# Kernel tuning notes

Measured on AMD Instinct MI355X. Metric: run time of the kernel, lower is better.

Reference implementation:

```python
import jax, jax.numpy as jnp
import numpy as np

N_NODES = 100000
N_EDGES = 1600000
IN_DIM = 512
OUT_DIM = 64


def setup_inputs() -> dict:
    key = jax.random.key(0)
    k1, k2, k3 = jax.random.split(key, 3)
    x = jax.random.normal(k1, (N_NODES, IN_DIM), dtype=jnp.float32)
    edge_index = jax.random.randint(k2, (2, N_EDGES), 0, N_NODES, dtype=jnp.int64)
    # Glorot-ish init for the GCNConv linear weight, stored as [in, out]
    W = jax.random.normal(k3, (IN_DIM, OUT_DIM), dtype=jnp.float32) * (1.0 / np.sqrt(IN_DIM))
    b = jnp.zeros((OUT_DIM,), dtype=jnp.float32)
    return {"x": x, "edge_index": edge_index, "W": W, "b": b}


def reference(x, edge_index, W, b):
    N = x.shape[0]
    # --- gcn_norm: add self-loops, symmetric degree normalization ---
    loop = jnp.arange(N, dtype=edge_index.dtype)
    src = jnp.concatenate([edge_index[0], loop])  # message sources
    dst = jnp.concatenate([edge_index[1], loop])  # aggregation targets
    deg = jax.ops.segment_sum(jnp.ones_like(dst, dtype=x.dtype), dst, num_segments=N)
    deg_inv_sqrt = jnp.where(deg > 0, jax.lax.rsqrt(jnp.maximum(deg, 1.0)), 0.0)
    norm = deg_inv_sqrt[src] * deg_inv_sqrt[dst]  # [E+N]
    # --- linear transform then gather-scale-scatter aggregation ---
    h = x @ W                                   # [N, out]
    msg = h[src] * norm[:, None]                # [E+N, out]
    out = jax.ops.segment_sum(msg, dst, num_segments=N) + b
    return jax.nn.log_softmax(out, axis=1)
```

## Files before the change

### kernel.cpp

```cpp
#include <hip/hip_runtime.h>
#include <math.h>

#define N_NODES 100000
#define N_EDGES 1600000
#define IN_DIM 512
#define OUT_DIM 64
#define NB 1024
#define NPB 128
#define CHUNK (N_EDGES / NPB)
#define N_BUCKETS_USED 782
#define N_TILES (N_NODES / 16)
#define GEMM_WAVES 4096

typedef __attribute__((ext_vector_type(8))) short short8;
typedef __attribute__((ext_vector_type(4))) float float4v;

__device__ __forceinline__ unsigned short f2bf(float f) {
    unsigned int u = __float_as_uint(f);
    u += 0x7fffu + ((u >> 16) & 1u);
    return (unsigned short)(u >> 16);
}
__device__ __forceinline__ float bf2f(unsigned short s) {
    return __uint_as_float(((unsigned int)s) << 16);
}
__device__ __forceinline__ short8 cvt8(float4v lo, float4v hi) {
    union { short8 s8; unsigned short us[8]; } af;
    af.us[0] = f2bf(lo.x); af.us[1] = f2bf(lo.y);
    af.us[2] = f2bf(lo.z); af.us[3] = f2bf(lo.w);
    af.us[4] = f2bf(hi.x); af.us[5] = f2bf(hi.y);
    af.us[6] = f2bf(hi.z); af.us[7] = f2bf(hi.w);
    return af.s8;
}

__global__ __launch_bounds__(256) void k_hist1(const int* __restrict__ dst,
                                               int* __restrict__ blockHist) {
    __shared__ int hist[NB];
    const int t = threadIdx.x, b = blockIdx.x;
    for (int k = t; k < NB; k += 256) hist[k] = 0;
    __syncthreads();
    const int e0 = b * CHUNK;
    for (int i = t; i < CHUNK; i += 256)
        atomicAdd(&hist[dst[e0 + i] >> 7], 1);
    __syncthreads();
    for (int k = t; k < NB; k += 256) blockHist[b * NB + k] = hist[k];
}

__global__ __launch_bounds__(256) void k_offsets(const int* __restrict__ blockHist,
                                                 int* __restrict__ blockStart,
                                                 int* __restrict__ bucketBase) {
    __shared__ int colsum[NB];
    __shared__ int bbase[NB + 1];
    __shared__ int wtot[4];
    const int t = threadIdx.x, lane = t & 63, w = t >> 6;
    for (int k = t; k < NB; k += 256) {
        int s = 0;
        for (int b = 0; b < NPB; ++b) s += blockHist[b * NB + k];
        colsum[k] = s;
    }
    __syncthreads();
    int c0 = colsum[t * 4 + 0], c1 = colsum[t * 4 + 1];
    int c2 = colsum[t * 4 + 2], c3 = colsum[t * 4 + 3];
    int tsum = c0 + c1 + c2 + c3;
    int incl = tsum;
#pragma unroll
    for (int off = 1; off < 64; off <<= 1) {
        int u = __shfl_up(incl, off, 64);
        if (lane >= off) incl += u;
    }
    if (lane == 63) wtot[w] = incl;
    __syncthreads();
    int woff = 0;
#pragma unroll
    for (int k2 = 0; k2 < 4; ++k2) if (k2 < w) woff += wtot[k2];
    int excl = woff + incl - tsum;
    bbase[t * 4 + 0] = excl;
    bbase[t * 4 + 1] = excl + c0;
    bbase[t * 4 + 2] = excl + c0 + c1;
    bbase[t * 4 + 3] = excl + c0 + c1 + c2;
    if (t == 255) bbase[NB] = excl + tsum;
    __syncthreads();
    for (int k = t; k < NB + 1; k += 256) bucketBase[k] = bbase[k];
    for (int k = t; k < NB; k += 256) {
        int run = bbase[k];
        for (int b = 0; b < NPB; ++b) {
            blockStart[b * NB + k] = run;
            run += blockHist[b * NB + k];
        }
    }
}

__global__ __launch_bounds__(256) void k_partition(const int* __restrict__ dst,
                                                   const int* __restrict__ src,
                                                   const int* __restrict__ blockStart,
                                                   int* __restrict__ parts) {
    __shared__ int cursor[NB];
    const int t = threadIdx.x, b = blockIdx.x;
    for (int k = t; k < NB; k += 256) cursor[k] = blockStart[b * NB + k];
    __syncthreads();
    const int e0 = b * CHUNK;
    for (int i = t; i < CHUNK; i += 256) {
        int d = dst[e0 + i];
        int s = src[e0 + i];
        int k = d >> 7;
        int pos = atomicAdd(&cursor[k], 1);
        parts[pos] = ((d & 127) << 17) | s;
    }
}

__global__ __launch_bounds__(256) void k_bucket(const int* __restrict__ parts,
                                                const int* __restrict__ bucketBase,
                                                int* __restrict__ degi,
                                                int* __restrict__ row_ptr,
                                                int* __restrict__ csr) {
    __shared__ int cnt[128];
    __shared__ int cur[128];
    __shared__ int wtot[2];
    const int t = threadIdx.x, k = blockIdx.x;
    const int base = bucketBase[k];
    const int n    = bucketBase[k + 1] - base;
    if (t < 128) cnt[t] = 0;
    __syncthreads();
    for (int i = t; i < n; i += 256)
        atomicAdd(&cnt[parts[base + i] >> 17], 1);
    __syncthreads();
    int incl = 0, v = 0;
    if (t < 128) {
        int lane = t & 63;
        v = cnt[t];
        incl = v;
#pragma unroll
        for (int off = 1; off < 64; off <<= 1) {
            int u = __shfl_up(incl, off, 64);
            if (lane >= off) incl += u;
        }
        if (lane == 63) wtot[t >> 6] = incl;
    }
    __syncthreads();
    if (t < 128) {
        int excl = incl - v + ((t >> 6) ? wtot[0] : 0);
        cur[t] = excl;
        int node = k * 128 + t;
        if (node < N_NODES) {
            degi[node]    = v;
            row_ptr[node] = base + excl;
        }
    }
    __syncthreads();
    for (int i = t; i < n; i += 256) {
        int code = parts[base + i];
        int nl = code >> 17, s = code & 0x1FFFF;
        int pos = atomicAdd(&cur[nl], 1);
        csr[base + pos] = s;
    }
}

__global__ __launch_bounds__(256) void k_wswz(const float* __restrict__ W,
                                              unsigned short* __restrict__ Wswz) {
    int t = blockIdx.x * 256 + threadIdx.x;
    if (t < IN_DIM * OUT_DIM) {
        int k = t >> 6, n = t & 63;
        int kt = k >> 5, kin = k & 31;
        int quad = kin >> 3, j = kin & 7;
        int ct = n >> 4, l16 = n & 15;
        int lane = quad * 16 + l16;
        Wswz[(((kt * 4 + ct) * 64 + lane) * 8) + j] = f2bf(W[t]);
    }
}

__global__ __launch_bounds__(512, 2) void k_gemm(const float* __restrict__ x,
                                              const unsigned short* __restrict__ Wswz,
                                              const int* __restrict__ degi,
                                              unsigned short* __restrict__ h) {
    __shared__ short8 Wlds[64][64];
    const int t = threadIdx.x;
    {
        const float4v* s = (const float4v*)Wswz;
        float4v* d = (float4v*)Wlds;
        for (int i = t; i < 4096; i += 512) d[i] = s[i];
    }
    __syncthreads();

    const int lane = t & 63;
    const int quad = lane >> 4, l16 = lane & 15;
    const int wid = blockIdx.x * 8 + (t >> 6);

    const int t0 = (int)(((long)wid * N_TILES) / GEMM_WAVES);
    const int t1 = (int)(((long)(wid + 1) * N_TILES) / GEMM_WAVES);

    for (int tile = t0; tile < t1; ++tile) {
        const int r0 = tile * 16;
        const float* xrow = x + (size_t)(r0 + l16) * IN_DIM + quad * 8;

        float4v plo[4], phi[4];
#pragma unroll
        for (int kt = 0; kt < 4; ++kt) {
            plo[kt] = *(const float4v*)(xrow + kt * 32);
            phi[kt] = *(const float4v*)(xrow + kt * 32 + 4);
        }
        float4v acc[4] = {{0.f,0.f,0.f,0.f},{0.f,0.f,0.f,0.f},
                          {0.f,0.f,0.f,0.f},{0.f,0.f,0.f,0.f}};

#pragma unroll 1
        for (int kq = 0; kq < 4; ++kq) {
            short8 A[4];
#pragma unroll
            for (int kt = 0; kt < 4; ++kt) A[kt] = cvt8(plo[kt], phi[kt]);
            if (kq < 3) {
#pragma unroll
                for (int kt = 0; kt < 4; ++kt) {
                    plo[kt] = *(const float4v*)(xrow + (kq + 1) * 128 + kt * 32);
                    phi[kt] = *(const float4v*)(xrow + (kq + 1) * 128 + kt * 32 + 4);
                }
            }
#pragma unroll
            for (int kt = 0; kt < 4; ++kt) {
#pragma unroll
                for (int ct = 0; ct < 4; ++ct) {
                    short8 bf = Wlds[(kq * 4 + kt) * 4 + ct][lane];
                    acc[ct] = __builtin_amdgcn_mfma_f32_16x16x32_bf16(A[kt], bf, acc[ct], 0, 0, 0);
                }
            }
        }

#pragma unroll
        for (int reg = 0; reg < 4; ++reg) {
            int orow = r0 + quad * 4 + reg;
            float dinv = rsqrtf((float)(degi[orow] + 1));
#pragma unroll
            for (int ct = 0; ct < 4; ++ct)
                h[(size_t)orow * OUT_DIM + ct * 16 + l16] = f2bf(acc[ct][reg] * dinv);
        }
    }
}

__global__ __launch_bounds__(256) void k_gather(const int* __restrict__ degi,
                                                const int* __restrict__ row_ptr,
                                                const int* __restrict__ csr,
                                                const unsigned short* __restrict__ h,
                                                const float* __restrict__ b,
                                                float* __restrict__ out) {
    int node = blockIdx.x * 4 + (threadIdx.x >> 6);
    int lane = threadIdx.x & 63;
    if (node >= N_NODES) return;
    int cnt  = __builtin_amdgcn_readfirstlane(degi[node]);
    int base = __builtin_amdgcn_readfirstlane(row_ptr[node]);

    float acc = bf2f(h[(size_t)node * OUT_DIM + lane]);
    int e = 0;
    for (; e + 8 <= cnt; e += 8) {
        int s0 = csr[base + e + 0], s1 = csr[base + e + 1];
        int s2 = csr[base + e + 2], s3 = csr[base + e + 3];
        int s4 = csr[base + e + 4], s5 = csr[base + e + 5];
        int s6 = csr[base + e + 6], s7 = csr[base + e + 7];
        float v0 = bf2f(h[(size_t)s0 * OUT_DIM + lane]);
        float v1 = bf2f(h[(size_t)s1 * OUT_DIM + lane]);
        float v2 = bf2f(h[(size_t)s2 * OUT_DIM + lane]);
        float v3 = bf2f(h[(size_t)s3 * OUT_DIM + lane]);
        float v4 = bf2f(h[(size_t)s4 * OUT_DIM + lane]);
        float v5 = bf2f(h[(size_t)s5 * OUT_DIM + lane]);
        float v6 = bf2f(h[(size_t)s6 * OUT_DIM + lane]);
        float v7 = bf2f(h[(size_t)s7 * OUT_DIM + lane]);
        acc += ((v0 + v1) + (v2 + v3)) + ((v4 + v5) + (v6 + v7));
    }
    for (; e < cnt; ++e)
        acc += bf2f(h[(size_t)csr[base + e] * OUT_DIM + lane]);

    float v = acc * rsqrtf((float)(cnt + 1)) + b[lane];
    float m = v;
#pragma unroll
    for (int off = 32; off > 0; off >>= 1) m = fmaxf(m, __shfl_xor(m, off, 64));
    float ex = expf(v - m);
    float s = ex;
#pragma unroll
    for (int off = 32; off > 0; off >>= 1) s += __shfl_xor(s, off, 64);
    out[(size_t)node * OUT_DIM + lane] = v - m - logf(s);
}

extern "C" void kernel_launch(void* const* d_in, const int* in_sizes, int n_in,
                              void* d_out, int out_size, void* d_ws, size_t ws_size,
                              hipStream_t stream) {
    const float* x  = (const float*)d_in[0];
    const int*   ei = (const int*)d_in[1];
    const float* W  = (const float*)d_in[2];
    const float* b  = (const float*)d_in[3];
    float* out = (float*)d_out;

    char* ws = (char*)d_ws;
    int*            degi       = (int*)(ws + 0);
    int*            row_ptr    = (int*)(ws + 400000);
    int*            blockHist  = (int*)(ws + 800000);
    int*            blockStart = (int*)(ws + 1324288);
    int*            bucketBase = (int*)(ws + 1848576);
    unsigned short* Wswz       = (unsigned short*)(ws + 1852928);
    unsigned short* h          = (unsigned short*)(ws + 1918464);
    int*            parts      = (int*)(ws + 14718464);
    int*            csr        = (int*)(ws + 21118464);

    const int* src = ei;
    const int* dst = ei + N_EDGES;

    k_hist1    <<<NPB, 256, 0, stream>>>(dst, blockHist);
    k_offsets  <<<1,   256, 0, stream>>>(blockHist, blockStart, bucketBase);
    k_partition<<<NPB, 256, 0, stream>>>(dst, src, blockStart, parts);
    k_bucket   <<<N_BUCKETS_USED, 256, 0, stream>>>(parts, bucketBase, degi, row_ptr, csr);
    k_wswz     <<<(IN_DIM * OUT_DIM + 255) / 256, 256, 0, stream>>>(W, Wswz);
    k_gemm     <<<512, 512, 0, stream>>>(x, Wswz, degi, h);
    k_gather   <<<(N_NODES + 3) / 4, 256, 0, stream>>>(degi, row_ptr, csr, h, b, out);
}
```

Measured before the change: 453.8 us.

## Stage x tiles into LDS with async double buffering and transpose block histogram

The GEMM now runs persistent 256 blocks over 128-row tiles. It streams x through double-buffered LDS using global_load_lds with an XOR swizzle, prefetching the next K-slice while MFMAs run on the current one. This replaces per-wave direct register loads. The block histogram layout is also transposed so k_offsets reads and writes contiguous rows with int4 loads. Risks include fewer waves per CU given 64KB of x buffer plus W in LDS, and a sync per K-slice.

```diff
diff --git a/kernel.cpp b/kernel.cpp
--- a/kernel.cpp
+++ b/kernel.cpp
@@ -9,8 +9,8 @@
 #define NPB 128
 #define CHUNK (N_EDGES / NPB)
 #define N_BUCKETS_USED 782
-#define N_TILES (N_NODES / 16)
-#define GEMM_WAVES 4096
+#define N_TILES128 782
+#define GEMM_BLOCKS 256
 
 typedef __attribute__((ext_vector_type(8))) short short8;
 typedef __attribute__((ext_vector_type(4))) float float4v;
@@ -31,6 +31,11 @@
     af.us[6] = f2bf(hi.z); af.us[7] = f2bf(hi.w);
     return af.s8;
 }
+__device__ __forceinline__ void gload_lds16(const void* g, void* lds) {
+    __builtin_amdgcn_global_load_lds(
+        (const __attribute__((address_space(1))) unsigned int*)g,
+        (__attribute__((address_space(3))) unsigned int*)lds, 16, 0, 0);
+}
 
 __global__ __launch_bounds__(256) void k_hist1(const int* __restrict__ dst,
                                                int* __restrict__ blockHist) {
@@ -42,7 +47,7 @@
     for (int i = t; i < CHUNK; i += 256)
         atomicAdd(&hist[dst[e0 + i] >> 7], 1);
     __syncthreads();
-    for (int k = t; k < NB; k += 256) blockHist[b * NB + k] = hist[k];
+    for (int k = t; k < NB; k += 256) blockHist[k * NPB + b] = hist[k];
 }
 
 __global__ __launch_bounds__(256) void k_offsets(const int* __restrict__ blockHist,
@@ -53,8 +58,13 @@
     __shared__ int wtot[4];
     const int t = threadIdx.x, lane = t & 63, w = t >> 6;
     for (int k = t; k < NB; k += 256) {
+        const int4* p = (const int4*)(blockHist + k * NPB);
         int s = 0;
-        for (int b = 0; b < NPB; ++b) s += blockHist[b * NB + k];
+#pragma unroll
+        for (int j = 0; j < NPB / 4; ++j) {
+            int4 v = p[j];
+            s += v.x + v.y + v.z + v.w;
+        }
         colsum[k] = s;
     }
     __syncthreads();
@@ -82,9 +92,11 @@
     for (int k = t; k < NB + 1; k += 256) bucketBase[k] = bbase[k];
     for (int k = t; k < NB; k += 256) {
         int run = bbase[k];
+        const int* ph = blockHist + k * NPB;
+        int* ps = blockStart + k * NPB;
         for (int b = 0; b < NPB; ++b) {
-            blockStart[b * NB + k] = run;
-            run += blockHist[b * NB + k];
+            ps[b] = run;
+            run += ph[b];
         }
     }
 }
@@ -95,7 +107,7 @@
                                                    int* __restrict__ parts) {
     __shared__ int cursor[NB];
     const int t = threadIdx.x, b = blockIdx.x;
-    for (int k = t; k < NB; k += 256) cursor[k] = blockStart[b * NB + k];
+    for (int k = t; k < NB; k += 256) cursor[k] = blockStart[k * NPB + b];
     __syncthreads();
     const int e0 = b * CHUNK;
     for (int i = t; i < CHUNK; i += 256) {
@@ -167,69 +179,91 @@
     }
 }
 
-__global__ __launch_bounds__(512, 2) void k_gemm(const float* __restrict__ x,
+__global__ __launch_bounds__(512) void k_gemm(const float* __restrict__ x,
                                               const unsigned short* __restrict__ Wswz,
                                               const int* __restrict__ degi,
                                               unsigned short* __restrict__ h) {
     __shared__ short8 Wlds[64][64];
+    __shared__ float  xbuf[2][8192];
     const int t = threadIdx.x;
     {
         const float4v* s = (const float4v*)Wswz;
         float4v* d = (float4v*)Wlds;
         for (int i = t; i < 4096; i += 512) d[i] = s[i];
     }
-    __syncthreads();
 
     const int lane = t & 63;
+    const int w    = t >> 6;
     const int quad = lane >> 4, l16 = lane & 15;
-    const int wid = blockIdx.x * 8 + (t >> 6);
-
-    const int t0 = (int)(((long)wid * N_TILES) / GEMM_WAVES);
-    const int t1 = (int)(((long)(wid + 1) * N_TILES) / GEMM_WAVES);
-
-    for (int tile = t0; tile < t1; ++tile) {
-        const int r0 = tile * 16;
-        const float* xrow = x + (size_t)(r0 + l16) * IN_DIM + quad * 8;
-
-        float4v plo[4], phi[4];
-#pragma unroll
-        for (int kt = 0; kt < 4; ++kt) {
-            plo[kt] = *(const float4v*)(xrow + kt * 32);
-            phi[kt] = *(const float4v*)(xrow + kt * 32 + 4);
-        }
+
+    int p0[4], prow[4], pwin[4];
+#pragma unroll
+    for (int c = 0; c < 4; ++c) {
+        int p = (w * 4 + c) * 1024 + lane * 16;
+        p0[c] = p;
+        int r = p >> 8;
+        prow[c] = r;
+        pwin[c] = (p & 255) ^ ((r & 7) << 4);
+    }
+
+    auto STAGE = [&](int rowBase, int s, int buf) {
+#pragma unroll
+        for (int c = 0; c < 4; ++c) {
+            int rg = rowBase + prow[c];
+            rg = rg < N_NODES ? rg : (N_NODES - 1);
+            const float* g = x + (size_t)rg * IN_DIM + s * 64 + (pwin[c] >> 2);
+            char* lp = ((char*)xbuf) + buf * 32768 + p0[c];
+            gload_lds16(g, lp);
+        }
+    };
+
+    const int rl   = w * 16 + l16;
+    const int sw   = (rl & 7) << 4;
+    const int rb   = rl * 256;
+
+    int tile = blockIdx.x;
+    STAGE(tile * 128, 0, 0);
+    __syncthreads();
+
+    while (true) {
+        const int rowBase = tile * 128;
         float4v acc[4] = {{0.f,0.f,0.f,0.f},{0.f,0.f,0.f,0.f},
                           {0.f,0.f,0.f,0.f},{0.f,0.f,0.f,0.f}};
-
 #pragma unroll 1
-        for (int kq = 0; kq < 4; ++kq) {
-            short8 A[4];
-#pragma unroll
-            for (int kt = 0; kt < 4; ++kt) A[kt] = cvt8(plo[kt], phi[kt]);
-            if (kq < 3) {
-#pragma unroll
-                for (int kt = 0; kt < 4; ++kt) {
-                    plo[kt] = *(const float4v*)(xrow + (kq + 1) * 128 + kt * 32);
-                    phi[kt] = *(const float4v*)(xrow + (kq + 1) * 128 + kt * 32 + 4);
+        for (int s = 0; s < 8; ++s) {
+            if (s < 7) {
+                STAGE(rowBase, s + 1, (s + 1) & 1);
+            } else {
+                int nt = tile + GEMM_BLOCKS;
+                if (nt < N_TILES128) STAGE(nt * 128, 0, 0);
+            }
+            const char* Xb = ((const char*)xbuf) + (s & 1) * 32768;
+#pragma unroll
+            for (int kt = 0; kt < 2; ++kt) {
+                int boff = rb + ((kt * 128 + quad * 32) ^ sw);
+                float4v lo = *(const float4v*)(Xb + boff);
+                float4v hi = *(const float4v*)(Xb + (boff ^ 16));
+                short8 a = cvt8(lo, hi);
+#pragma unroll
+                for (int ct = 0; ct < 4; ++ct) {
+                    short8 bf = Wlds[(s * 2 + kt) * 4 + ct][lane];
+                    acc[ct] = __builtin_amdgcn_mfma_f32_16x16x32_bf16(a, bf, acc[ct], 0, 0, 0);
                 }
             }
-#pragma unroll
-            for (int kt = 0; kt < 4; ++kt) {
-#pragma unroll
-                for (int ct = 0; ct < 4; ++ct) {
-                    short8 bf = Wlds[(kq * 4 + kt) * 4 + ct][lane];
-                    acc[ct] = __builtin_amdgcn_mfma_f32_16x16x32_bf16(A[kt], bf, acc[ct], 0, 0, 0);
-                }
+            __syncthreads();
+        }
+#pragma unroll
+        for (int reg = 0; reg < 4; ++reg) {
+            int orow = rowBase + w * 16 + quad * 4 + reg;
+            if (orow < N_NODES) {
+                float dinv = rsqrtf((float)(degi[orow] + 1));
+#pragma unroll
+                for (int ct = 0; ct < 4; ++ct)
+                    h[(size_t)orow * OUT_DIM + ct * 16 + l16] = f2bf(acc[ct][reg] * dinv);
             }
         }
-
-#pragma unroll
-        for (int reg = 0; reg < 4; ++reg) {
-            int orow = r0 + quad * 4 + reg;
-            float dinv = rsqrtf((float)(degi[orow] + 1));
-#pragma unroll
-            for (int ct = 0; ct < 4; ++ct)
-                h[(size_t)orow * OUT_DIM + ct * 16 + l16] = f2bf(acc[ct][reg] * dinv);
-        }
+        tile += GEMM_BLOCKS;
+        if (tile >= N_TILES128) break;
     }
 }
 
@@ -304,6 +338,6 @@
     k_partition<<<NPB, 256, 0, stream>>>(dst, src, blockStart, parts);
     k_bucket   <<<N_BUCKETS_USED, 256, 0, stream>>>(parts, bucketBase, degi, row_ptr, csr);
     k_wswz     <<<(IN_DIM * OUT_DIM + 255) / 256, 256, 0, stream>>>(W, Wswz);
-    k_gemm     <<<512, 512, 0, stream>>>(x, Wswz, degi, h);
+    k_gemm     <<<GEMM_BLOCKS, 512, 0, stream>>>(x, Wswz, degi, h);
     k_gather   <<<(N_NODES + 3) / 4, 256, 0, stream>>>(degi, row_ptr, csr, h, b, out);
 }
```

Result: slower. 478.9 us (+5.5%).

## Split gather wavefront into four edge groups with 8-byte row loads

Applied to the files above, without the earlier changes.

The per-node gather now has each group of 16 lanes handle a different edge, loading 4 bf16 features per lane as a uint2. This replaces one 2-byte load per lane with four edges fetched in parallel per wavefront. The partial sums are combined with cross-lane shuffles before a shortened log-softmax, and only lanes 0-15 write the output with float4 stores. The aim is more memory-level parallelism and fewer load instructions per edge, at the cost of extra shuffles and idle lanes during the epilogue.

```diff
diff --git a/kernel.cpp b/kernel.cpp
--- a/kernel.cpp
+++ b/kernel.cpp
@@ -22,6 +22,12 @@
 }
 __device__ __forceinline__ float bf2f(unsigned short s) {
     return __uint_as_float(((unsigned int)s) << 16);
+}
+__device__ __forceinline__ float bf2f_lo(unsigned int u) {
+    return __uint_as_float(u << 16);
+}
+__device__ __forceinline__ float bf2f_hi(unsigned int u) {
+    return __uint_as_float(u & 0xffff0000u);
 }
 __device__ __forceinline__ short8 cvt8(float4v lo, float4v hi) {
     union { short8 s8; unsigned short us[8]; } af;
@@ -242,38 +248,60 @@
     int node = blockIdx.x * 4 + (threadIdx.x >> 6);
     int lane = threadIdx.x & 63;
     if (node >= N_NODES) return;
+    const int sub = lane >> 4;
+    const int c4  = lane & 15;
     int cnt  = __builtin_amdgcn_readfirstlane(degi[node]);
     int base = __builtin_amdgcn_readfirstlane(row_ptr[node]);
 
-    float acc = bf2f(h[(size_t)node * OUT_DIM + lane]);
-    int e = 0;
-    for (; e + 8 <= cnt; e += 8) {
-        int s0 = csr[base + e + 0], s1 = csr[base + e + 1];
-        int s2 = csr[base + e + 2], s3 = csr[base + e + 3];
-        int s4 = csr[base + e + 4], s5 = csr[base + e + 5];
-        int s6 = csr[base + e + 6], s7 = csr[base + e + 7];
-        float v0 = bf2f(h[(size_t)s0 * OUT_DIM + lane]);
-        float v1 = bf2f(h[(size_t)s1 * OUT_DIM + lane]);
-        float v2 = bf2f(h[(size_t)s2 * OUT_DIM + lane]);
-        float v3 = bf2f(h[(size_t)s3 * OUT_DIM + lane]);
-        float v4 = bf2f(h[(size_t)s4 * OUT_DIM + lane]);
-        float v5 = bf2f(h[(size_t)s5 * OUT_DIM + lane]);
-        float v6 = bf2f(h[(size_t)s6 * OUT_DIM + lane]);
-        float v7 = bf2f(h[(size_t)s7 * OUT_DIM + lane]);
-        acc += ((v0 + v1) + (v2 + v3)) + ((v4 + v5) + (v6 + v7));
-    }
-    for (; e < cnt; ++e)
-        acc += bf2f(h[(size_t)csr[base + e] * OUT_DIM + lane]);
-
-    float v = acc * rsqrtf((float)(cnt + 1)) + b[lane];
-    float m = v;
-#pragma unroll
-    for (int off = 32; off > 0; off >>= 1) m = fmaxf(m, __shfl_xor(m, off, 64));
-    float ex = expf(v - m);
-    float s = ex;
-#pragma unroll
-    for (int off = 32; off > 0; off >>= 1) s += __shfl_xor(s, off, 64);
-    out[(size_t)node * OUT_DIM + lane] = v - m - logf(s);
+    float a0 = 0.f, a1 = 0.f, a2 = 0.f, a3 = 0.f;
+    if (sub == 0) {
+        uint2 v = *(const uint2*)(h + (size_t)node * OUT_DIM + c4 * 4);
+        a0 = bf2f_lo(v.x); a1 = bf2f_hi(v.x);
+        a2 = bf2f_lo(v.y); a3 = bf2f_hi(v.y);
+    }
+
+    int e = sub;
+    for (; e + 4 < cnt; e += 8) {
+        int s0 = csr[base + e];
+        int s1 = csr[base + e + 4];
+        uint2 va = *(const uint2*)(h + (size_t)s0 * OUT_DIM + c4 * 4);
+        uint2 vb = *(const uint2*)(h + (size_t)s1 * OUT_DIM + c4 * 4);
+        a0 += bf2f_lo(va.x) + bf2f_lo(vb.x);
+        a1 += bf2f_hi(va.x) + bf2f_hi(vb.x);
+        a2 += bf2f_lo(va.y) + bf2f_lo(vb.y);
+        a3 += bf2f_hi(va.y) + bf2f_hi(vb.y);
+    }
+    if (e < cnt) {
+        int s0 = csr[base + e];
+        uint2 va = *(const uint2*)(h + (size_t)s0 * OUT_DIM + c4 * 4);
+        a0 += bf2f_lo(va.x); a1 += bf2f_hi(va.x);
+        a2 += bf2f_lo(va.y); a3 += bf2f_hi(va.y);
+    }
+
+    a0 += __shfl_xor(a0, 16, 64); a0 += __shfl_xor(a0, 32, 64);
+    a1 += __shfl_xor(a1, 16, 64); a1 += __shfl_xor(a1, 32, 64);
+    a2 += __shfl_xor(a2, 16, 64); a2 += __shfl_xor(a2, 32, 64);
+    a3 += __shfl_xor(a3, 16, 64); a3 += __shfl_xor(a3, 32, 64);
+
+    float dinv = rsqrtf((float)(cnt + 1));
+    const float4v bb = *(const float4v*)(b + c4 * 4);
+    float v0 = a0 * dinv + bb.x;
+    float v1 = a1 * dinv + bb.y;
+    float v2 = a2 * dinv + bb.z;
+    float v3 = a3 * dinv + bb.w;
+
+    float m = fmaxf(fmaxf(v0, v1), fmaxf(v2, v3));
+#pragma unroll
+    for (int off = 1; off < 16; off <<= 1) m = fmaxf(m, __shfl_xor(m, off, 64));
+    float s = expf(v0 - m) + expf(v1 - m) + expf(v2 - m) + expf(v3 - m);
+#pragma unroll
+    for (int off = 1; off < 16; off <<= 1) s += __shfl_xor(s, off, 64);
+    float ls = m + logf(s);
+
+    if (sub == 0) {
+        float4v r = {v0 - ls, v1 - ls, v2 - ls, v3 - ls};
+        *(float4v*)(out + (size_t)node * OUT_DIM + c4 * 4) = r;
+    }
 }
 
 extern "C" void kernel_launch(void* const* d_in, const int* in_sizes, int n_in,
```

After: 455.7 us. About the same (+0.4%).
